# Optimization experiments

Measured on AMD Instinct MI355X. Metric: run time of the kernel, lower is better.

Reference implementation:

```python
import jax, jax.numpy as jnp
import numpy as np

N_NODES = 20000
N_EDGES = 320000
N_RELS = 500
EMB = 256
D4 = EMB // 4
B = 32
GAMMA = 12.0
BN_EPS = 1e-5


def _linear(x, W, b):
    return x @ W.T + b


def _bn(x, g, b, m, v):
    # BatchNorm1d in eval mode with running stats
    return (x - m) * jax.lax.rsqrt(v + BN_EPS) * g + b


def _comp_layer(src, dst, h, e, WO, bO, WI, bI, WS, bS, bng, bnb, bnm, bnv):
    # CompGCNLayer: u_sub_e message + per-node mean over in-edges ('ho')
    # and, on the reversed graph, over out-edges ('hi'); nodes with no
    # incident edges get 0 (dgl mean semantics).
    n = h.shape[0]
    ones = jnp.ones(src.shape[0], h.dtype)
    deg_in = jnp.maximum(jax.ops.segment_sum(ones, dst, num_segments=n), 1.0)
    deg_out = jnp.maximum(jax.ops.segment_sum(ones, src, num_segments=n), 1.0)
    ho = jax.ops.segment_sum(h[src] - e, dst, num_segments=n) / deg_in[:, None]
    hi = jax.ops.segment_sum(h[dst] - e, src, num_segments=n) / deg_out[:, None]
    out = (_linear(ho, WO, bO) + _linear(hi, WI, bI) + _linear(h, WS, bS)) / 3.0
    return _bn(out, bng, bnb, bnm, bnv)


def _forward(node_embs, edge_embs, params, src, dst, e_vid, hids, rids, tids,
             is_update_g_embs, is_head_pred):
    (W_O1, b_O1, W_I1, b_I1, W_S1, b_S1, bn1_g, bn1_b, bn1_m, bn1_v, Wr1, br1,
     W_O2, b_O2, W_I2, b_I2, W_S2, b_S2, bn2_g, bn2_b, bn2_m, bn2_v, Wr2, br2) = params
    if is_update_g_embs:
        he = edge_embs[e_vid]                                   # [E, D]
        h1 = jnp.tanh(_comp_layer(src, dst, node_embs, he,
                                  W_O1, b_O1, W_I1, b_I1, W_S1, b_S1,
                                  bn1_g, bn1_b, bn1_m, bn1_v))  # [N, D/4]
        he1 = jnp.tanh(_linear(he, Wr1, br1))                   # [E, D/4]
        hn = jnp.tanh(_comp_layer(src, dst, h1, he1,
                                  W_O2, b_O2, W_I2, b_I2, W_S2, b_S2,
                                  bn2_g, bn2_b, bn2_m, bn2_v))  # [N, D]
    else:
        hn = node_embs
    heads = hn[hids]
    tails = hn[tids]
    rels = _linear(jax.nn.relu(_linear(edge_embs[rids], Wr1, br1)), Wr2, br2)
    b = hids.shape[0]
    n = hn.shape[0]
    # Faithful to torch repeat_interleave indexing in predict():
    # flat element k pairs query row k//C with candidate row k//B.
    cand_idx = (jnp.arange(b)[:, None] * n + jnp.arange(n)[None, :]) // b  # [B, N]
    cand = hn[cand_idx]                                                    # [B, N, D]
    if is_head_pred == 1:
        diff = cand + (rels - tails)[:, None, :]
    else:
        diff = (heads + rels)[:, None, :] - cand
    dist = jnp.sqrt(jnp.sum(diff * diff, axis=-1))  # p = norm = 2
    score = jax.nn.sigmoid(GAMMA - dist)
    return hn, score


def setup_inputs() -> dict:
    key = jax.random.key(0)
    ks = jax.random.split(key, 20)
    w = lambda k, shp: jax.random.normal(k, shp, jnp.float32) * 0.05
    inp = {
        "node_embs": jax.random.normal(ks[0], (N_NODES, EMB), jnp.float32),
        "edge_embs": jax.random.normal(ks[1], (N_RELS, EMB), jnp.float32),
        "W_O1": w(ks[2], (D4, EMB)), "b_O1": jnp.zeros((D4,), jnp.float32),
        "W_I1": w(ks[3], (D4, EMB)), "b_I1": jnp.zeros((D4,), jnp.float32),
        "W_S1": w(ks[4], (D4, EMB)), "b_S1": jnp.zeros((D4,), jnp.float32),
        "bn1_g": jnp.ones((D4,), jnp.float32), "bn1_b": jnp.zeros((D4,), jnp.float32),
        "bn1_m": jnp.zeros((D4,), jnp.float32), "bn1_v": jnp.ones((D4,), jnp.float32),
        "Wr1": w(ks[5], (D4, EMB)), "br1": jnp.zeros((D4,), jnp.float32),
        "W_O2": w(ks[6], (EMB, D4)), "b_O2": jnp.zeros((EMB,), jnp.float32),
        "W_I2": w(ks[7], (EMB, D4)), "b_I2": jnp.zeros((EMB,), jnp.float32),
        "W_S2": w(ks[8], (EMB, D4)), "b_S2": jnp.zeros((EMB,), jnp.float32),
        "bn2_g": jnp.ones((EMB,), jnp.float32), "bn2_b": jnp.zeros((EMB,), jnp.float32),
        "bn2_m": jnp.zeros((EMB,), jnp.float32), "bn2_v": jnp.ones((EMB,), jnp.float32),
        "Wr2": w(ks[9], (EMB, D4)), "br2": jnp.zeros((EMB,), jnp.float32),
        "src": jax.random.randint(ks[10], (N_EDGES,), 0, N_NODES, jnp.int32),
        "dst": jax.random.randint(ks[11], (N_EDGES,), 0, N_NODES, jnp.int32),
        "e_vid": jax.random.randint(ks[12], (N_EDGES,), 0, N_RELS, jnp.int32),
        "hids": jax.random.randint(ks[13], (B,), 0, N_NODES, jnp.int32),
        "rids": jax.random.randint(ks[14], (B,), 0, N_RELS, jnp.int32),
        "tids": jax.random.randint(ks[15], (B,), 0, N_NODES, jnp.int32),
        "is_update_g_embs": 1,
        "is_head_pred": 0,
    }
    return inp


def reference(node_embs, edge_embs,
              W_O1, b_O1, W_I1, b_I1, W_S1, b_S1, bn1_g, bn1_b, bn1_m, bn1_v,
              Wr1, br1,
              W_O2, b_O2, W_I2, b_I2, W_S2, b_S2, bn2_g, bn2_b, bn2_m, bn2_v,
              Wr2, br2,
              src, dst, e_vid, hids, rids, tids,
              is_update_g_embs, is_head_pred):
    params = (W_O1, b_O1, W_I1, b_I1, W_S1, b_S1, bn1_g, bn1_b, bn1_m, bn1_v,
              Wr1, br1,
              W_O2, b_O2, W_I2, b_I2, W_S2, b_S2, bn2_g, bn2_b, bn2_m, bn2_v,
              Wr2, br2)
    return _forward(node_embs, edge_embs, params, src, dst, e_vid,
                    hids, rids, tids, is_update_g_embs, is_head_pred)
```

## Files before the change

### kernel.cpp

```cpp
#include <hip/hip_runtime.h>
#include <math.h>

#define NN 20000
#define NE 320000
#define NR 500
#define EMBD 256
#define D4 64
#define BQ 32
#define TOT (2 * NN)
#define NB 40

#define NBLK_HIST 1250
#define NBLK_BN 448
#define NBLK_K1 (NBLK_HIST + NBLK_BN + 2 + BQ)

#define NBLK_GC1 939
#define NBLK_GE1 32
#define NBLK_MEGA (NBLK_HIST + NBLK_GE1 + NBLK_GC1)

typedef __attribute__((ext_vector_type(8))) short bf16x8;
typedef __attribute__((ext_vector_type(4))) float f32x4;

__device__ __forceinline__ unsigned short f2bf(float x)
{
    unsigned int u = __float_as_uint(x);
    unsigned int r = (u + 0x7fffu + ((u >> 16) & 1u)) >> 16;
    return (unsigned short)r;
}

__device__ __forceinline__ float4 bf4tof4(uint2 u)
{
    float4 r;
    r.x = __uint_as_float((u.x & 0xFFFFu) << 16);
    r.y = __uint_as_float(u.x & 0xFFFF0000u);
    r.z = __uint_as_float((u.y & 0xFFFFu) << 16);
    r.w = __uint_as_float(u.y & 0xFFFF0000u);
    return r;
}

__global__ __launch_bounds__(256) void k_prep(
    const int* __restrict__ src, const int* __restrict__ dst,
    int* __restrict__ cnt, unsigned* __restrict__ rank2,
    const float* __restrict__ W_O1, const float* __restrict__ W_I1,
    const float* __restrict__ W_S1, const float* __restrict__ Wr1,
    const float* __restrict__ W_O2, const float* __restrict__ W_I2,
    const float* __restrict__ W_S2,
    unsigned short* __restrict__ Bn1, unsigned short* __restrict__ Bn2,
    const float* __restrict__ bO1, const float* __restrict__ bI1,
    const float* __restrict__ bS1,
    const float* __restrict__ g1, const float* __restrict__ bb1,
    const float* __restrict__ m1, const float* __restrict__ v1,
    const float* __restrict__ bO2, const float* __restrict__ bI2,
    const float* __restrict__ bS2,
    const float* __restrict__ g2, const float* __restrict__ bb2,
    const float* __restrict__ m2, const float* __restrict__ v2,
    float* __restrict__ s1, float* __restrict__ t1,
    float* __restrict__ s2, float* __restrict__ t2,
    const float* __restrict__ edge_embs,
    const float* __restrict__ br1, const float* __restrict__ br2,
    const float* __restrict__ Wr2full, const int* __restrict__ rids,
    float* __restrict__ rels)
{
    int b = blockIdx.x;
    if (b < NBLK_HIST) {
        int i = b * 256 + threadIdx.x;
        if (i < NE) {
            int r_in = atomicAdd(&cnt[dst[i]], 1);
            int r_out = atomicAdd(&cnt[NN + src[i]], 1);
            rank2[i] = (unsigned)r_in | ((unsigned)r_out << 16);
        }
        return;
    }
    b -= NBLK_HIST;
    if (b < NBLK_BN) {
        int id = b * 256 + threadIdx.x;
        if (id < 256 * 256) {
            int n = id >> 8, k = id & 255;
            float v;
            if (n < 64)       v = W_O1[n * 256 + k];
            else if (n < 128) v = W_I1[(n - 64) * 256 + k];
            else if (n < 192) v = W_S1[(n - 128) * 256 + k];
            else              v = Wr1[(n - 192) * 256 + k];
            Bn1[id] = f2bf(v);
        } else {
            int id2 = id - 256 * 256;
            if (id2 < 256 * 192) {
                int n = id2 / 192, k = id2 - n * 192;
                float v;
                if (k < 64)       v = W_O2[n * 64 + k];
                else if (k < 128) v = W_I2[n * 64 + (k - 64)];
                else              v = W_S2[n * 64 + (k - 128)];
                Bn2[id2] = f2bf(v);
            }
        }
        return;
    }
    b -= NBLK_BN;
    if (b < 2) {
        int i = b * 256 + threadIdx.x;
        if (i < 64) {
            float rsg = g1[i] / sqrtf(v1[i] + 1e-5f);
            s1[i] = rsg * (1.f / 3.f);
            t1[i] = ((bO1[i] + bI1[i] + bS1[i]) * (1.f / 3.f) - m1[i]) * rsg + bb1[i];
        } else if (i < 320) {
            int n = i - 64;
            float rsg = g2[n] / sqrtf(v2[n] + 1e-5f);
            s2[n] = rsg * (1.f / 3.f);
            t2[n] = ((bO2[n] + bI2[n] + bS2[n]) * (1.f / 3.f) - m2[n]) * rsg + bb2[n];
        }
        return;
    }
    {
        __shared__ float e_s[256];
        __shared__ float m_s[64];
        int rb = b - 2, o = threadIdx.x;
        int rid = rids[rb];
        e_s[o] = edge_embs[(size_t)rid * 256 + o];
        __syncthreads();
        if (o < 64) {
            float acc = br1[o];
            for (int k = 0; k < 256; ++k) acc = fmaf(e_s[k], Wr1[o * 256 + k], acc);
            m_s[o] = fmaxf(acc, 0.f);
        }
        __syncthreads();
        float r = br2[o];
        for (int jj = 0; jj < 64; ++jj) r = fmaf(m_s[jj], Wr2full[o * 64 + jj], r);
        rels[rb * 256 + o] = r;
    }
}

__global__ __launch_bounds__(256) void k_scan(const int* __restrict__ cnt,
                                              int* __restrict__ off_bin,
                                              int* __restrict__ bsum,
                                              int* __restrict__ flag)
{
    __shared__ int lds[256];
    __shared__ int pre_s;
    int t = threadIdx.x, bid = blockIdx.x;
    int base = bid * 1024 + t * 4;
    int e0 = 0, e1 = 0, e2 = 0, e3 = 0;
    if (base + 3 < TOT) {
        int4 v = *(const int4*)(cnt + base);
        e0 = v.x; e1 = v.y; e2 = v.z; e3 = v.w;
    } else {
        if (base + 0 < TOT) e0 = cnt[base + 0];
        if (base + 1 < TOT) e1 = cnt[base + 1];
        if (base + 2 < TOT) e2 = cnt[base + 2];
        if (base + 3 < TOT) e3 = cnt[base + 3];
    }
    int s = e0 + e1 + e2 + e3;
    lds[t] = s;
    __syncthreads();
    for (int d = 1; d < 256; d <<= 1) {
        int u = (t >= d) ? lds[t - d] : 0;
        __syncthreads();
        lds[t] += u;
        __syncthreads();
    }
    if (t == 255) {
        bsum[bid] = lds[255];
        __threadfence();
        atomicAdd(flag, 1);
    }
    if (t == 0) {
        while (atomicAdd(flag, 0) < NB) { }
    }
    __syncthreads();
    __threadfence();
    if (t < 64) {
        int v = (t < bid) ? atomicAdd(&bsum[t], 0) : 0;
#pragma unroll
        for (int d = 32; d >= 1; d >>= 1) v += __shfl_xor(v, d, 64);
        if (t == 0) pre_s = v;
    }
    __syncthreads();
    int run = lds[t] - s + pre_s;
    if (base + 3 < TOT) {
        int4 o = make_int4(run, run + e0, run + e0 + e1, run + e0 + e1 + e2);
        *(int4*)(off_bin + base) = o;
    } else {
        int r = run;
        if (base + 0 < TOT) { off_bin[base + 0] = r; r += e0; }
        if (base + 1 < TOT) { off_bin[base + 1] = r; r += e1; }
        if (base + 2 < TOT) { off_bin[base + 2] = r; r += e2; }
        if (base + 3 < TOT) { off_bin[base + 3] = r; r += e3; }
    }
    if (bid == 0 && t == 0) off_bin[TOT] = 2 * NE;
}

__device__ __forceinline__ void gemm_dev(
    unsigned short* As, unsigned short* Bs,
    const void* __restrict__ Av, int aBf16, int M, int K, int lda,
    const unsigned short* __restrict__ Bn,
    void* __restrict__ C, int ldc, int mode,
    const float* __restrict__ sv, const float* __restrict__ tv,
    const float* __restrict__ node_embs, const int* __restrict__ flag,
    int m0, int n0)
{
    const int t = threadIdx.x;
    const int lane = t & 63, wave = t >> 6;
    const int wr = wave >> 1, wc = wave & 1;
    const int lrow = lane & 15, lkg = lane >> 4;

    f32x4 acc[2][2] = {};

    for (int kb = 0; kb < K; kb += 64) {
        if (aBf16) {
            const unsigned short* A = (const unsigned short*)Av;
#pragma unroll
            for (int it = 0; it < 2; ++it) {
                int idx = t + it * 256;
                int ko = idx & 7;
                int row = idx >> 3;
                int gm = m0 + row;
                uint4 a = make_uint4(0u, 0u, 0u, 0u);
                if (gm < M) a = *(const uint4*)(A + (size_t)gm * lda + kb + 8 * ko);
                *(uint4*)&As[row * 72 + 8 * ko] = a;
            }
        } else {
            const float* A = (const float*)Av;
#pragma unroll
            for (int it = 0; it < 4; ++it) {
                int idx = t + it * 256;
                int kq = idx & 15;
                int row = idx >> 4;
                int gm = m0 + row;
                float4 a = make_float4(0.f, 0.f, 0.f, 0.f);
                if (gm < M) a = *(const float4*)(A + (size_t)gm * lda + kb + 4 * kq);
                unsigned int p0 = (unsigned int)f2bf(a.x) | ((unsigned int)f2bf(a.y) << 16);
                unsigned int p1 = (unsigned int)f2bf(a.z) | ((unsigned int)f2bf(a.w) << 16);
                *(uint2*)&As[row * 72 + 4 * kq] = make_uint2(p0, p1);
            }
        }
#pragma unroll
        for (int it = 0; it < 2; ++it) {
            int idx = t + it * 256;
            int ko = idx & 7;
            int row = idx >> 3;
            uint4 b = *(const uint4*)(Bn + (size_t)(n0 + row) * K + kb + 8 * ko);
            *(uint4*)&Bs[row * 72 + 8 * ko] = b;
        }
        __syncthreads();
#pragma unroll
        for (int ks = 0; ks < 2; ++ks) {
            int k0 = ks * 32 + lkg * 8;
            bf16x8 af0 = *(const bf16x8*)&As[(wr * 32 + lrow) * 72 + k0];
            bf16x8 af1 = *(const bf16x8*)&As[(wr * 32 + 16 + lrow) * 72 + k0];
            bf16x8 bf0 = *(const bf16x8*)&Bs[(wc * 32 + lrow) * 72 + k0];
            bf16x8 bf1 = *(const bf16x8*)&Bs[(wc * 32 + 16 + lrow) * 72 + k0];
            acc[0][0] = __builtin_amdgcn_mfma_f32_16x16x32_bf16(af0, bf0, acc[0][0], 0, 0, 0);
            acc[0][1] = __builtin_amdgcn_mfma_f32_16x16x32_bf16(af0, bf1, acc[0][1], 0, 0, 0);
            acc[1][0] = __builtin_amdgcn_mfma_f32_16x16x32_bf16(af1, bf0, acc[1][0], 0, 0, 0);
            acc[1][1] = __builtin_amdgcn_mfma_f32_16x16x32_bf16(af1, bf1, acc[1][1], 0, 0, 0);
        }
        __syncthreads();
    }

#pragma unroll
    for (int m = 0; m < 2; ++m) {
#pragma unroll
        for (int r = 0; r < 4; ++r) {
            int gm = m0 + wr * 32 + m * 16 + lkg * 4 + r;
            if (gm >= M) continue;
#pragma unroll
            for (int n = 0; n < 2; ++n) {
                int gn = n0 + wc * 32 + n * 16 + lrow;
                float v = acc[m][n][r];
                if (mode == 0) {
                    ((unsigned short*)C)[(size_t)gm * ldc + gn] = f2bf(v);
                } else if (mode == 1) {
                    float val = (gn >= 192) ? tanhf(v + sv[gn - 192]) : v;
                    ((unsigned short*)C)[(size_t)gm * ldc + gn] = f2bf(val);
                } else {
                    float val = tanhf(v * sv[gn] + tv[gn]);
                    if (flag[0] == 0) val = node_embs[(size_t)gm * EMBD + gn];
                    ((float*)C)[(size_t)gm * EMBD + gn] = val;
                }
            }
        }
    }
}

__global__ __launch_bounds__(256) void gemm_mfma(
    const void* __restrict__ A, int aBf16, int M, int K, int lda,
    const unsigned short* __restrict__ Bn,
    void* __restrict__ C, int ldc, int mode,
    const float* __restrict__ sv, const float* __restrict__ tv,
    const float* __restrict__ node_embs, const int* __restrict__ flag)
{
    __shared__ unsigned short As[64 * 72];
    __shared__ unsigned short Bs[64 * 72];
    gemm_dev(As, Bs, A, aBf16, M, K, lda, Bn, C, ldc, mode, sv, tv, node_embs, flag,
             blockIdx.x * 64, blockIdx.y * 64);
}

__global__ __launch_bounds__(256) void k_mega(
    const float* __restrict__ node_embs, const float* __restrict__ edge_embs,
    const unsigned short* __restrict__ Bn1,
    unsigned short* __restrict__ C1b, unsigned short* __restrict__ E1b,
    const float* __restrict__ br1,
    const int* __restrict__ src, const int* __restrict__ dst,
    const int* __restrict__ evid, const unsigned* __restrict__ rank2,
    const int* __restrict__ offc, unsigned* __restrict__ R)
{
    __shared__ unsigned short As[64 * 72];
    __shared__ unsigned short Bs[64 * 72];
    int bid = blockIdx.x;
    if (bid < NBLK_HIST) {
        int e = bid * 256 + threadIdx.x;
        if (e < NE) {
            int s = src[e], d = dst[e];
            unsigned rv = (unsigned)evid[e] << 15;
            unsigned rk = rank2[e];
            R[offc[d] + (rk & 0xFFFFu)] = (unsigned)s | rv;
            R[offc[NN + s] + (rk >> 16)] = (unsigned)d | rv;
        }
        return;
    }
    int b2 = bid - NBLK_HIST;
    if (b2 < NBLK_GE1) {
        gemm_dev(As, Bs, edge_embs, 0, NR, 256, 256, Bn1, E1b, 256, 1,
                 br1, nullptr, nullptr, nullptr,
                 (b2 % 8) * 64, (b2 / 8) * 64);
    } else {
        int b3 = b2 - NBLK_GE1;
        gemm_dev(As, Bs, node_embs, 0, NN, 256, 256, Bn1, C1b, 192, 0,
                 nullptr, nullptr, nullptr, nullptr,
                 (b3 % 313) * 64, (b3 / 313) * 64);
    }
}


__device__ __forceinline__ void gather_quad(
    const unsigned* __restrict__ R, int r0, int r1, int g, int q,
    const unsigned short* __restrict__ TAB, int ldt, int toff,
    const unsigned short* __restrict__ ETAB, int eoff,
    float4& acc)
{
    int lane = g * 16 + q;
    int cnt = r1 - r0;
    for (int base = 0; base < cnt; base += 64) {
        int rem = cnt - base; if (rem > 64) rem = 64;
        unsigned rec = 0u;
        if (lane < rem) rec = R[r0 + base + lane];
        int i = 0;
        for (; 4 * i + 15 < rem; i += 4) {
            unsigned ra = __shfl(rec, 4 * i + g, 64);
            unsigned rb = __shfl(rec, 4 * i + 4 + g, 64);
            unsigned rc = __shfl(rec, 4 * i + 8 + g, 64);
            unsigned rd = __shfl(rec, 4 * i + 12 + g, 64);
            uint2 ua0 = *(const uint2*)(TAB + (size_t)(ra & 0x7FFFu) * ldt + toff + 4 * q);
            uint2 ue0 = *(const uint2*)(ETAB + (size_t)(ra >> 15) * 256 + eoff + 4 * q);
            uint2 ua1 = *(const uint2*)(TAB + (size_t)(rb & 0x7FFFu) * ldt + toff + 4 * q);
            uint2 ue1 = *(const uint2*)(ETAB + (size_t)(rb >> 15) * 256 + eoff + 4 * q);
            uint2 ua2 = *(const uint2*)(TAB + (size_t)(rc & 0x7FFFu) * ldt + toff + 4 * q);
            uint2 ue2 = *(const uint2*)(ETAB + (size_t)(rc >> 15) * 256 + eoff + 4 * q);
            uint2 ua3 = *(const uint2*)(TAB + (size_t)(rd & 0x7FFFu) * ldt + toff + 4 * q);
            uint2 ue3 = *(const uint2*)(ETAB + (size_t)(rd >> 15) * 256 + eoff + 4 * q);
            float4 a0 = bf4tof4(ua0), e0 = bf4tof4(ue0);
            float4 a1 = bf4tof4(ua1), e1 = bf4tof4(ue1);
            float4 a2 = bf4tof4(ua2), e2 = bf4tof4(ue2);
            float4 a3 = bf4tof4(ua3), e3 = bf4tof4(ue3);
            acc.x += (a0.x - e0.x) + (a1.x - e1.x) + (a2.x - e2.x) + (a3.x - e3.x);
            acc.y += (a0.y - e0.y) + (a1.y - e1.y) + (a2.y - e2.y) + (a3.y - e3.y);
            acc.z += (a0.z - e0.z) + (a1.z - e1.z) + (a2.z - e2.z) + (a3.z - e3.z);
            acc.w += (a0.w - e0.w) + (a1.w - e1.w) + (a2.w - e2.w) + (a3.w - e3.w);
        }
        for (; 4 * i < rem; ++i) {
            int idx = 4 * i + g;
            unsigned rr = __shfl(rec, idx < rem ? idx : 0, 64);
            if (idx < rem) {
                uint2 ua = *(const uint2*)(TAB + (size_t)(rr & 0x7FFFu) * ldt + toff + 4 * q);
                uint2 ue = *(const uint2*)(ETAB + (size_t)(rr >> 15) * 256 + eoff + 4 * q);
                float4 a = bf4tof4(ua), e = bf4tof4(ue);
                acc.x += a.x - e.x; acc.y += a.y - e.y;
                acc.z += a.z - e.z; acc.w += a.w - e.w;
            }
        }
    }
}

__device__ __forceinline__ void xreduce(float4& v)
{
    v.x += __shfl_xor(v.x, 16, 64); v.y += __shfl_xor(v.y, 16, 64);
    v.z += __shfl_xor(v.z, 16, 64); v.w += __shfl_xor(v.w, 16, 64);
    v.x += __shfl_xor(v.x, 32, 64); v.y += __shfl_xor(v.y, 32, 64);
    v.z += __shfl_xor(v.z, 32, 64); v.w += __shfl_xor(v.w, 32, 64);
}

__device__ __forceinline__ uint2 packbf4(float4 o)
{
    return make_uint2((unsigned)f2bf(o.x) | ((unsigned)f2bf(o.y) << 16),
                      (unsigned)f2bf(o.z) | ((unsigned)f2bf(o.w) << 16));
}

__global__ __launch_bounds__(256) void k_gather1(
    const int* __restrict__ offc, const unsigned* __restrict__ R,
    const unsigned short* __restrict__ C1b, const unsigned short* __restrict__ E1b,
    const float* __restrict__ s1, const float* __restrict__ t1,
    unsigned short* __restrict__ A2b)
{
    int n = blockIdx.x * 4 + (threadIdx.x >> 6);
    if (n >= NN) return;
    int lane = threadIdx.x & 63, g = lane >> 4, q = lane & 15;
    int b0 = offc[n], b1 = offc[n + 1];
    int c0 = offc[NN + n], c1 = offc[NN + n + 1];
    float di = 1.f / fmaxf((float)(b1 - b0), 1.f);
    float dh = 1.f / fmaxf((float)(c1 - c0), 1.f);
    float4 accO = make_float4(0.f, 0.f, 0.f, 0.f);
    float4 accI = make_float4(0.f, 0.f, 0.f, 0.f);
    gather_quad(R, b0, b1, g, q, C1b, 192, 0, E1b, 0, accO);
    gather_quad(R, c0, c1, g, q, C1b, 192, 64, E1b, 64, accI);
    xreduce(accO);
    xreduce(accI);
    if (g == 0) {
        float4 hs = bf4tof4(*(const uint2*)(C1b + (size_t)n * 192 + 128 + 4 * q));
        float4 sv = *(const float4*)(s1 + 4 * q);
        float4 tv = *(const float4*)(t1 + 4 * q);
        float4 o;
        o.x = tanhf((accO.x * di + accI.x * dh + hs.x) * sv.x + tv.x);
        o.y = tanhf((accO.y * di + accI.y * dh + hs.y) * sv.y + tv.y);
        o.z = tanhf((accO.z * di + accI.z * dh + hs.z) * sv.z + tv.z);
        o.w = tanhf((accO.w * di + accI.w * dh + hs.w) * sv.w + tv.w);
        *(uint2*)(A2b + (size_t)n * 192 + 128 + 4 * q) = packbf4(o);
    }
}

__global__ __launch_bounds__(256) void k_gather2(
    const int* __restrict__ offc, const unsigned* __restrict__ R,
    const unsigned short* __restrict__ A2r, const unsigned short* __restrict__ E1b,
    unsigned short* __restrict__ A2w)
{
    int n = blockIdx.x * 4 + (threadIdx.x >> 6);
    if (n >= NN) return;
    int lane = threadIdx.x & 63, g = lane >> 4, q = lane & 15;
    int b0 = offc[n], b1 = offc[n + 1];
    int c0 = offc[NN + n], c1 = offc[NN + n + 1];
    float di = 1.f / fmaxf((float)(b1 - b0), 1.f);
    float dh = 1.f / fmaxf((float)(c1 - c0), 1.f);
    float4 accO = make_float4(0.f, 0.f, 0.f, 0.f);
    float4 accI = make_float4(0.f, 0.f, 0.f, 0.f);
    gather_quad(R, b0, b1, g, q, A2r, 192, 128, E1b, 192, accO);
    gather_quad(R, c0, c1, g, q, A2r, 192, 128, E1b, 192, accI);
    xreduce(accO);
    xreduce(accI);
    if (g == 0) {
        float4 o0, o1;
        o0.x = accO.x * di; o0.y = accO.y * di; o0.z = accO.z * di; o0.w = accO.w * di;
        o1.x = accI.x * dh; o1.y = accI.y * dh; o1.z = accI.z * dh; o1.w = accI.w * dh;
        *(uint2*)(A2w + (size_t)n * 192 + 4 * q) = packbf4(o0);
        *(uint2*)(A2w + (size_t)n * 192 + 64 + 4 * q) = packbf4(o1);
    }
}

__global__ __launch_bounds__(256) void k_score(
    const float* __restrict__ hn, const float* __restrict__ rels,
    const int* __restrict__ hids, const int* __restrict__ tids,
    const int* __restrict__ is_head, float* __restrict__ score)
{
    int p = blockIdx.x * 4 + (threadIdx.x >> 6);
    if (p >= BQ * (NN / BQ)) return;
    int l = threadIdx.x & 63;
    int b = p / (NN / BQ);
    int j = p - b * (NN / BQ);
    int idx = (b * NN + 32 * j) / BQ;
    int ih = is_head[0];
    int nid = ih ? tids[b] : hids[b];
    float ssum = 0.f;
#pragma unroll
    for (int q = 0; q < 4; ++q) {
        float r = rels[b * 256 + l + 64 * q];
        float hv = hn[(size_t)nid * 256 + l + 64 * q];
        float tv = ih ? (hv - r) : (hv + r);
        float df = hn[(size_t)idx * 256 + l + 64 * q] - tv;
        ssum = fmaf(df, df, ssum);
    }
#pragma unroll
    for (int off = 32; off >= 1; off >>= 1) ssum += __shfl_xor(ssum, off, 64);
    float dist = sqrtf(ssum);
    float sc = 1.f / (1.f + expf(dist - 12.f));
    if (l < 32) score[(size_t)b * NN + 32 * j + l] = sc;
}

extern "C" void kernel_launch(void* const* d_in, const int* in_sizes, int n_in,
                              void* d_out, int out_size, void* d_ws, size_t ws_size,
                              hipStream_t stream)
{
    const float* node_embs = (const float*)d_in[0];
    const float* edge_embs = (const float*)d_in[1];
    const float* W_O1 = (const float*)d_in[2];  const float* b_O1 = (const float*)d_in[3];
    const float* W_I1 = (const float*)d_in[4];  const float* b_I1 = (const float*)d_in[5];
    const float* W_S1 = (const float*)d_in[6];  const float* b_S1 = (const float*)d_in[7];
    const float* bn1_g = (const float*)d_in[8]; const float* bn1_b = (const float*)d_in[9];
    const float* bn1_m = (const float*)d_in[10];const float* bn1_v = (const float*)d_in[11];
    const float* Wr1 = (const float*)d_in[12];  const float* br1 = (const float*)d_in[13];
    const float* W_O2 = (const float*)d_in[14]; const float* b_O2 = (const float*)d_in[15];
    const float* W_I2 = (const float*)d_in[16]; const float* b_I2 = (const float*)d_in[17];
    const float* W_S2 = (const float*)d_in[18]; const float* b_S2 = (const float*)d_in[19];
    const float* bn2_g = (const float*)d_in[20];const float* bn2_b = (const float*)d_in[21];
    const float* bn2_m = (const float*)d_in[22];const float* bn2_v = (const float*)d_in[23];
    const float* Wr2 = (const float*)d_in[24];  const float* br2 = (const float*)d_in[25];
    const int* src = (const int*)d_in[26];
    const int* dst = (const int*)d_in[27];
    const int* evid = (const int*)d_in[28];
    const int* hids = (const int*)d_in[29];
    const int* rids = (const int*)d_in[30];
    const int* tids = (const int*)d_in[31];
    const int* upd = (const int*)d_in[32];
    const int* ihead = (const int*)d_in[33];

    unsigned short* C1b = (unsigned short*)d_ws;
    unsigned short* A2b = C1b + 3840000;
    unsigned short* E1b = A2b + 3840000;
    unsigned short* Bn1 = E1b + 128000;
    unsigned short* Bn2 = Bn1 + 65536;

    float* s1   = (float*)(Bn2 + 49152);
    float* t1   = s1 + 64;
    float* s2   = t1 + 64;
    float* t2   = s2 + 256;
    float* rels = t2 + 256;

    unsigned* R     = (unsigned*)(rels + 8192);
    unsigned* rank2 = R + 2 * NE;
    int* cnt    = (int*)(rank2 + NE);
    int* flag   = cnt + TOT;
    int* off_bin= flag + 1;
    int* bsum   = off_bin + TOT + 1;

    float* hn    = (float*)d_out;
    float* score = hn + (size_t)NN * EMBD;

    hipMemsetAsync(cnt, 0, (size_t)(TOT + 1) * 4, stream);

    k_prep<<<NBLK_K1, 256, 0, stream>>>(
        src, dst, cnt, rank2,
        W_O1, W_I1, W_S1, Wr1, W_O2, W_I2, W_S2, Bn1, Bn2,
        b_O1, b_I1, b_S1, bn1_g, bn1_b, bn1_m, bn1_v,
        b_O2, b_I2, b_S2, bn2_g, bn2_b, bn2_m, bn2_v,
        s1, t1, s2, t2,
        edge_embs, br1, br2, Wr2, rids, rels);

    k_scan<<<NB, 256, 0, stream>>>(cnt, off_bin, bsum, flag);

    k_mega<<<NBLK_MEGA, 256, 0, stream>>>(node_embs, edge_embs, Bn1,
                                          C1b, E1b, br1, src, dst, evid, rank2, off_bin, R);

    k_gather1<<<NN / 4, 256, 0, stream>>>(off_bin, R, C1b, E1b, s1, t1, A2b);
    k_gather2<<<NN / 4, 256, 0, stream>>>(off_bin, R, A2b, E1b, A2b);

    gemm_mfma<<<dim3(313, 4), 256, 0, stream>>>(A2b, 1, NN, 192, 192, Bn2,
                                                hn, 256, 2, s2, t2, node_embs, upd);

    k_score<<<(BQ * (NN / BQ)) / 4, 256, 0, stream>>>(hn, rels, hids, tids, ihead, score);
}
```

Baseline: 144.5 us.

## Interleave in/out CSR segments per node and merge the two gather passes

Counts and offsets are now interleaved per node (in-edges then out-edges contiguous), and each record carries a direction bit. The two per-direction gather loops become one pass over a single contiguous range, with the accumulator and table offset chosen by that bit. This is meant to cut per-node loop overhead and tail waste for low-degree nodes. R stores and loads also become nontemporal. In exchange, the inner loop gains per-edge branching on direction. The scan producing offc must also match the new interleaved layout, and that part is not shown.

```diff
diff --git a/kernel.cpp b/kernel.cpp
--- a/kernel.cpp
+++ b/kernel.cpp
@@ -65,8 +65,8 @@
     if (b < NBLK_HIST) {
         int i = b * 256 + threadIdx.x;
         if (i < NE) {
-            int r_in = atomicAdd(&cnt[dst[i]], 1);
-            int r_out = atomicAdd(&cnt[NN + src[i]], 1);
+            int r_in = atomicAdd(&cnt[2 * dst[i]], 1);
+            int r_out = atomicAdd(&cnt[2 * src[i] + 1], 1);
             rank2[i] = (unsigned)r_in | ((unsigned)r_out << 16);
         }
         return;
@@ -312,8 +312,10 @@
             int s = src[e], d = dst[e];
             unsigned rv = (unsigned)evid[e] << 15;
             unsigned rk = rank2[e];
-            R[offc[d] + (rk & 0xFFFFu)] = (unsigned)s | rv;
-            R[offc[NN + s] + (rk >> 16)] = (unsigned)d | rv;
+            __builtin_nontemporal_store((unsigned)s | rv,
+                                        &R[offc[2 * d] + (rk & 0xFFFFu)]);
+            __builtin_nontemporal_store((unsigned)d | rv | 0x80000000u,
+                                        &R[offc[2 * s + 1] + (rk >> 16)]);
         }
         return;
     }
@@ -331,50 +333,64 @@
 }
 
 
-__device__ __forceinline__ void gather_quad(
+__device__ __forceinline__ void gather_quad_m(
     const unsigned* __restrict__ R, int r0, int r1, int g, int q,
-    const unsigned short* __restrict__ TAB, int ldt, int toff,
-    const unsigned short* __restrict__ ETAB, int eoff,
-    float4& acc)
+    const unsigned short* __restrict__ TAB, int ldt, int toff0, int toff1,
+    const unsigned short* __restrict__ ETAB, int eoff0, int eoff1,
+    float4& accO, float4& accI)
 {
     int lane = g * 16 + q;
     int cnt = r1 - r0;
     for (int base = 0; base < cnt; base += 64) {
         int rem = cnt - base; if (rem > 64) rem = 64;
         unsigned rec = 0u;
-        if (lane < rem) rec = R[r0 + base + lane];
+        if (lane < rem) rec = __builtin_nontemporal_load(&R[r0 + base + lane]);
         int i = 0;
         for (; 4 * i + 15 < rem; i += 4) {
-            unsigned ra = __shfl(rec, 4 * i + g, 64);
-            unsigned rb = __shfl(rec, 4 * i + 4 + g, 64);
-            unsigned rc = __shfl(rec, 4 * i + 8 + g, 64);
-            unsigned rd = __shfl(rec, 4 * i + 12 + g, 64);
-            uint2 ua0 = *(const uint2*)(TAB + (size_t)(ra & 0x7FFFu) * ldt + toff + 4 * q);
-            uint2 ue0 = *(const uint2*)(ETAB + (size_t)(ra >> 15) * 256 + eoff + 4 * q);
-            uint2 ua1 = *(const uint2*)(TAB + (size_t)(rb & 0x7FFFu) * ldt + toff + 4 * q);
-            uint2 ue1 = *(const uint2*)(ETAB + (size_t)(rb >> 15) * 256 + eoff + 4 * q);
-            uint2 ua2 = *(const uint2*)(TAB + (size_t)(rc & 0x7FFFu) * ldt + toff + 4 * q);
-            uint2 ue2 = *(const uint2*)(ETAB + (size_t)(rc >> 15) * 256 + eoff + 4 * q);
-            uint2 ua3 = *(const uint2*)(TAB + (size_t)(rd & 0x7FFFu) * ldt + toff + 4 * q);
-            uint2 ue3 = *(const uint2*)(ETAB + (size_t)(rd >> 15) * 256 + eoff + 4 * q);
-            float4 a0 = bf4tof4(ua0), e0 = bf4tof4(ue0);
-            float4 a1 = bf4tof4(ua1), e1 = bf4tof4(ue1);
-            float4 a2 = bf4tof4(ua2), e2 = bf4tof4(ue2);
-            float4 a3 = bf4tof4(ua3), e3 = bf4tof4(ue3);
-            acc.x += (a0.x - e0.x) + (a1.x - e1.x) + (a2.x - e2.x) + (a3.x - e3.x);
-            acc.y += (a0.y - e0.y) + (a1.y - e1.y) + (a2.y - e2.y) + (a3.y - e3.y);
-            acc.z += (a0.z - e0.z) + (a1.z - e1.z) + (a2.z - e2.z) + (a3.z - e3.z);
-            acc.w += (a0.w - e0.w) + (a1.w - e1.w) + (a2.w - e2.w) + (a3.w - e3.w);
+            unsigned r4[4];
+            r4[0] = __shfl(rec, 4 * i + g, 64);
+            r4[1] = __shfl(rec, 4 * i + 4 + g, 64);
+            r4[2] = __shfl(rec, 4 * i + 8 + g, 64);
+            r4[3] = __shfl(rec, 4 * i + 12 + g, 64);
+            uint2 ua[4], ue[4];
+#pragma unroll
+            for (int u = 0; u < 4; ++u) {
+                unsigned rv = r4[u];
+                int dir = (int)(rv >> 31);
+                ua[u] = *(const uint2*)(TAB + (size_t)(rv & 0x7FFFu) * ldt +
+                                        (dir ? toff1 : toff0) + 4 * q);
+                ue[u] = *(const uint2*)(ETAB + (size_t)((rv >> 15) & 0x1FFu) * 256 +
+                                        (dir ? eoff1 : eoff0) + 4 * q);
+            }
+#pragma unroll
+            for (int u = 0; u < 4; ++u) {
+                float4 a = bf4tof4(ua[u]), e = bf4tof4(ue[u]);
+                if (r4[u] >> 31) {
+                    accI.x += a.x - e.x; accI.y += a.y - e.y;
+                    accI.z += a.z - e.z; accI.w += a.w - e.w;
+                } else {
+                    accO.x += a.x - e.x; accO.y += a.y - e.y;
+                    accO.z += a.z - e.z; accO.w += a.w - e.w;
+                }
+            }
         }
         for (; 4 * i < rem; ++i) {
             int idx = 4 * i + g;
             unsigned rr = __shfl(rec, idx < rem ? idx : 0, 64);
             if (idx < rem) {
-                uint2 ua = *(const uint2*)(TAB + (size_t)(rr & 0x7FFFu) * ldt + toff + 4 * q);
-                uint2 ue = *(const uint2*)(ETAB + (size_t)(rr >> 15) * 256 + eoff + 4 * q);
+                int dir = (int)(rr >> 31);
+                uint2 ua = *(const uint2*)(TAB + (size_t)(rr & 0x7FFFu) * ldt +
+                                           (dir ? toff1 : toff0) + 4 * q);
+                uint2 ue = *(const uint2*)(ETAB + (size_t)((rr >> 15) & 0x1FFu) * 256 +
+                                           (dir ? eoff1 : eoff0) + 4 * q);
                 float4 a = bf4tof4(ua), e = bf4tof4(ue);
-                acc.x += a.x - e.x; acc.y += a.y - e.y;
-                acc.z += a.z - e.z; acc.w += a.w - e.w;
+                if (dir) {
+                    accI.x += a.x - e.x; accI.y += a.y - e.y;
+                    accI.z += a.z - e.z; accI.w += a.w - e.w;
+                } else {
+                    accO.x += a.x - e.x; accO.y += a.y - e.y;
+                    accO.z += a.z - e.z; accO.w += a.w - e.w;
+                }
             }
         }
     }
@@ -403,14 +419,12 @@
     int n = blockIdx.x * 4 + (threadIdx.x >> 6);
     if (n >= NN) return;
     int lane = threadIdx.x & 63, g = lane >> 4, q = lane & 15;
-    int b0 = offc[n], b1 = offc[n + 1];
-    int c0 = offc[NN + n], c1 = offc[NN + n + 1];
-    float di = 1.f / fmaxf((float)(b1 - b0), 1.f);
-    float dh = 1.f / fmaxf((float)(c1 - c0), 1.f);
+    int b0 = offc[2 * n], bm = offc[2 * n + 1], b1 = offc[2 * n + 2];
+    float di = 1.f / fmaxf((float)(bm - b0), 1.f);
+    float dh = 1.f / fmaxf((float)(b1 - bm), 1.f);
     float4 accO = make_float4(0.f, 0.f, 0.f, 0.f);
     float4 accI = make_float4(0.f, 0.f, 0.f, 0.f);
-    gather_quad(R, b0, b1, g, q, C1b, 192, 0, E1b, 0, accO);
-    gather_quad(R, c0, c1, g, q, C1b, 192, 64, E1b, 64, accI);
+    gather_quad_m(R, b0, b1, g, q, C1b, 192, 0, 64, E1b, 0, 64, accO, accI);
     xreduce(accO);
     xreduce(accI);
     if (g == 0) {
@@ -434,14 +448,12 @@
     int n = blockIdx.x * 4 + (threadIdx.x >> 6);
     if (n >= NN) return;
     int lane = threadIdx.x & 63, g = lane >> 4, q = lane & 15;
-    int b0 = offc[n], b1 = offc[n + 1];
-    int c0 = offc[NN + n], c1 = offc[NN + n + 1];
-    float di = 1.f / fmaxf((float)(b1 - b0), 1.f);
-    float dh = 1.f / fmaxf((float)(c1 - c0), 1.f);
+    int b0 = offc[2 * n], bm = offc[2 * n + 1], b1 = offc[2 * n + 2];
+    float di = 1.f / fmaxf((float)(bm - b0), 1.f);
+    float dh = 1.f / fmaxf((float)(b1 - bm), 1.f);
     float4 accO = make_float4(0.f, 0.f, 0.f, 0.f);
     float4 accI = make_float4(0.f, 0.f, 0.f, 0.f);
-    gather_quad(R, b0, b1, g, q, A2r, 192, 128, E1b, 192, accO);
-    gather_quad(R, c0, c1, g, q, A2r, 192, 128, E1b, 192, accI);
+    gather_quad_m(R, b0, b1, g, q, A2r, 192, 128, 128, E1b, 192, 192, accO, accI);
     xreduce(accO);
     xreduce(accI);
     if (g == 0) {
```

New measurement: 144.4 us. About the same (-0.1%).
